# Kernel optimization log

Hardware: AMD Instinct MI355X
Metric: run time of the kernel (lower is better)

The kernel has to match this reference:

```python
import jax, jax.numpy as jnp
import numpy as np

N = 12                      # matrix size (input_size)
TRI = N * (N + 1) // 2      # 78 lower-triangular entries
HID = 512
BATCH = 262144


def setup_inputs() -> dict:
    key = jax.random.key(0)
    ks = jax.random.split(key, 4)
    s1 = 1.0 / np.sqrt(N)
    s2 = 1.0 / np.sqrt(HID)
    return {
        "x": jax.random.normal(ks[0], (BATCH, N), dtype=jnp.float32),
        "W1": jax.random.normal(ks[1], (N, HID), dtype=jnp.float32) * s1,
        "b1": jnp.zeros((HID,), dtype=jnp.float32),
        "W2": jax.random.normal(ks[2], (HID, HID), dtype=jnp.float32) * s2,
        "b2": jnp.zeros((HID,), dtype=jnp.float32),
        "W3": jax.random.normal(ks[3], (HID, TRI + 1), dtype=jnp.float32) * s2,
        "b3": jnp.zeros((TRI + 1,), dtype=jnp.float32),
    }


def reference(x, W1, b1, W2, b2, W3, b3):
    # 3-layer MLP (assumed parent-class structure): relu, relu, softplus
    h = jax.nn.relu(x @ W1 + b1)
    h = jax.nn.relu(h @ W2 + b2)
    out = jax.nn.softplus(h @ W3 + b3)          # [B, TRI+1]
    # Vectorized row-major lower-triangular scatter (replaces nested python loop)
    rows, cols = jnp.tril_indices(N)            # row-major order matches idx loop
    B = x.shape[0]
    L = jnp.zeros((B, N, N), dtype=out.dtype).at[:, rows, cols].set(out[:, :TRI])
    MMT = jnp.einsum('bij,bkj->bik', L, L)      # M @ M^T, PSD [B, N, N]
    c = out[:, TRI]                             # [B]
    return MMT, c
```

## Files before the change

kernel.cpp:

```cpp
#include <hip/hip_runtime.h>
#include <math.h>

typedef __attribute__((ext_vector_type(8))) _Float16 fp16x8;
typedef __attribute__((ext_vector_type(4))) _Float16 fp16x4;
typedef __attribute__((ext_vector_type(2))) __fp16 hfp16x2;
typedef __attribute__((ext_vector_type(4))) __fp16 hfp16x4;
typedef __attribute__((ext_vector_type(4))) float floatx4;

#define HID 512
#define TRIC 78
#define OUTC 79
#define BATCH 262144
#define HPAD 520
#define OPAD 84
#define XPAD 24
#define X_OFF 33280

#define W2P_OFF 16384
#define W3P_OFF 278528

__global__ __launch_bounds__(256) void prep_kernel(const float* __restrict__ W1,
                                                   const float* __restrict__ W2,
                                                   const float* __restrict__ W3,
                                                   _Float16* __restrict__ wsh) {
  int g = blockIdx.x * 256 + threadIdx.x;
  int lane = g & 63;
  int l15 = lane & 15, q = lane >> 4;
  fp16x8 v;
  if (g < 2048) {
    int ct = g >> 6;
    int c = ct * 16 + l15;
#pragma unroll
    for (int j = 0; j < 8; ++j) {
      int k = q * 8 + j;
      v[j] = (k < 12) ? (_Float16)W1[k * HID + c] : (_Float16)0.f;
    }
    *(fp16x8*)(wsh + (size_t)g * 8) = v;
  } else if (g < 34816) {
    int h = g - 2048;
    int fk = h >> 6;
    int kb = fk & 15, ct = fk >> 4;
    int c = ct * 16 + l15;
    int kbase = kb * 32 + q * 8;
#pragma unroll
    for (int j = 0; j < 8; ++j) v[j] = (_Float16)W2[(kbase + j) * HID + c];
    *(fp16x8*)(wsh + W2P_OFF + (size_t)h * 8) = v;
  } else if (g < 39936) {
    int h = g - 34816;
    int fk = h >> 6;
    int kb = fk & 15, ct = fk >> 4;
    int c = ct * 16 + l15;
    int kbase = kb * 32 + q * 8;
#pragma unroll
    for (int j = 0; j < 8; ++j)
      v[j] = (c < OUTC) ? (_Float16)W3[(kbase + j) * OUTC + c] : (_Float16)0.f;
    *(fp16x8*)(wsh + W3P_OFF + (size_t)h * 8) = v;
  }
}

__device__ __forceinline__ float softplus_f(float v) {
  float e = __expf(-fabsf(v));
  return fmaxf(v, 0.f) + __logf(1.f + e);
}

__device__ __forceinline__ fp16x4 relu_pk4(floatx4 a) {
  hfp16x2 lo = __builtin_amdgcn_cvt_pkrtz(fmaxf(a[0], 0.f), fmaxf(a[1], 0.f));
  hfp16x2 hi = __builtin_amdgcn_cvt_pkrtz(fmaxf(a[2], 0.f), fmaxf(a[3], 0.f));
  hfp16x4 r = __builtin_shufflevector(lo, hi, 0, 1, 2, 3);
  return __builtin_bit_cast(fp16x4, r);
}

__global__ __launch_bounds__(512, 4) void fused_kernel(const float* __restrict__ x,
                                                       const float* __restrict__ b1,
                                                       const float* __restrict__ b2,
                                                       const float* __restrict__ b3,
                                                       const _Float16* __restrict__ wsh,
                                                       float* __restrict__ out) {
  __shared__ __align__(16) _Float16 hbuf[X_OFF + 64 * XPAD];
  const int tid = threadIdx.x;
  const int wave = tid >> 6, lane = tid & 63;
  const int l15 = lane & 15, quad = lane >> 4;
  const int r0 = blockIdx.x * 64;

  const fp16x8* w1p = (const fp16x8*)wsh;
  const fp16x8* w2p = (const fp16x8*)(wsh + W2P_OFF);
  const fp16x8* w3p = (const fp16x8*)(wsh + W3P_OFF);

  {
    _Float16* xs = hbuf + X_OFF;
    const float* xg = x + (size_t)r0 * 12;
    if (tid < 256) {
      int e = 512 + tid;
      int row = e / 12, col = e - row * 12;
      xs[row * XPAD + col] = (_Float16)xg[e];
      xs[(tid >> 2) * XPAD + 12 + (tid & 3)] = (_Float16)0.f;
    }
    {
      int row = tid / 12, col = tid - row * 12;
      xs[row * XPAD + col] = (_Float16)xg[tid];
    }
  }
  fp16x8 a1p[4];
#pragma unroll
  for (int ct = 0; ct < 4; ++ct) a1p[ct] = w1p[(wave * 4 + ct) * 64 + lane];
  __syncthreads();

  fp16x8 zf;
#pragma unroll
  for (int j = 0; j < 8; ++j) zf[j] = (_Float16)0.f;

  floatx4 bq[4];
#pragma unroll
  for (int ct = 0; ct < 4; ++ct)
    bq[ct] = *(const floatx4*)(b1 + wave * 64 + ct * 16 + quad * 4);

  floatx4 acc[4][4];
#pragma unroll
  for (int ct = 0; ct < 4; ++ct)
#pragma unroll
    for (int nt = 0; nt < 4; ++nt) acc[ct][nt] = bq[ct];

  {
    const _Float16* xs = hbuf + X_OFF;
    fp16x8 xb[4];
#pragma unroll
    for (int nt = 0; nt < 4; ++nt)
      xb[nt] = (quad < 2) ? *(const fp16x8*)(xs + (nt * 16 + l15) * XPAD + quad * 8) : zf;
#pragma unroll
    for (int ct = 0; ct < 4; ++ct) {
#pragma unroll
      for (int nt = 0; nt < 4; ++nt)
        acc[ct][nt] = __builtin_amdgcn_mfma_f32_16x16x32_f16(a1p[ct], xb[nt], acc[ct][nt], 0, 0, 0);
    }
  }

#pragma unroll
  for (int ct = 0; ct < 4; ++ct)
#pragma unroll
    for (int nt = 0; nt < 4; ++nt)
      *(fp16x4*)(hbuf + (nt * 16 + l15) * HPAD + wave * 64 + ct * 16 + quad * 4) =
          relu_pk4(acc[ct][nt]);
  fp16x8 ap[4];
#pragma unroll
  for (int ct = 0; ct < 4; ++ct) ap[ct] = w2p[((wave * 4 + ct) * 16 + 0) * 64 + lane];
  __syncthreads();

#pragma unroll
  for (int ct = 0; ct < 4; ++ct)
    bq[ct] = *(const floatx4*)(b2 + wave * 64 + ct * 16 + quad * 4);
#pragma unroll
  for (int ct = 0; ct < 4; ++ct)
#pragma unroll
    for (int nt = 0; nt < 4; ++nt) acc[ct][nt] = bq[ct];

#pragma unroll 2
  for (int kb = 0; kb < 16; ++kb) {
    fp16x8 a[4], b[4];
#pragma unroll
    for (int ct = 0; ct < 4; ++ct) a[ct] = ap[ct];
#pragma unroll
    for (int nt = 0; nt < 4; ++nt)
      b[nt] = *(const fp16x8*)(hbuf + (nt * 16 + l15) * HPAD + kb * 32 + quad * 8);
    const int kbn = (kb + 1) & 15;
#pragma unroll
    for (int ct = 0; ct < 4; ++ct) ap[ct] = w2p[((wave * 4 + ct) * 16 + kbn) * 64 + lane];
    __builtin_amdgcn_s_setprio(1);
#pragma unroll
    for (int ct = 0; ct < 4; ++ct)
#pragma unroll
      for (int nt = 0; nt < 4; ++nt)
        acc[ct][nt] = __builtin_amdgcn_mfma_f32_16x16x32_f16(a[ct], b[nt], acc[ct][nt], 0, 0, 0);
    __builtin_amdgcn_s_setprio(0);
  }

  __syncthreads();

#pragma unroll
  for (int ct = 0; ct < 4; ++ct)
#pragma unroll
    for (int nt = 0; nt < 4; ++nt)
      *(fp16x4*)(hbuf + (nt * 16 + l15) * HPAD + wave * 64 + ct * 16 + quad * 4) =
          relu_pk4(acc[ct][nt]);

  const int mt3 = wave >> 1;
  const int codd = wave & 1;
  const int c0 = codd ? 3 : 0;
  const int nct = codd ? 2 : 3;

  floatx4 b3q[3];
#pragma unroll
  for (int j = 0; j < 3; ++j) {
#pragma unroll
    for (int r = 0; r < 4; ++r) {
      int c = (c0 + j) * 16 + quad * 4 + r;
      b3q[j][r] = (j < nct && c < OUTC) ? b3[c] : 0.f;
    }
  }
  floatx4 acc3[3];
#pragma unroll
  for (int j = 0; j < 3; ++j) acc3[j] = b3q[j];

  fp16x8 ap3[3];
#pragma unroll
  for (int j = 0; j < 3; ++j) ap3[j] = zf;
#pragma unroll
  for (int j = 0; j < 3; ++j)
    if (j < nct) ap3[j] = w3p[((c0 + j) * 16 + 0) * 64 + lane];
  __syncthreads();

#pragma unroll 2
  for (int kb = 0; kb < 16; ++kb) {
    fp16x8 bfrag = *(const fp16x8*)(hbuf + (mt3 * 16 + l15) * HPAD + kb * 32 + quad * 8);
    fp16x8 a3[3];
#pragma unroll
    for (int j = 0; j < 3; ++j) a3[j] = ap3[j];
    const int kbn = (kb + 1) & 15;
#pragma unroll
    for (int j = 0; j < 3; ++j)
      if (j < nct) ap3[j] = w3p[((c0 + j) * 16 + kbn) * 64 + lane];
    __builtin_amdgcn_s_setprio(1);
#pragma unroll
    for (int j = 0; j < 3; ++j)
      if (j < nct)
        acc3[j] = __builtin_amdgcn_mfma_f32_16x16x32_f16(a3[j], bfrag, acc3[j], 0, 0, 0);
    __builtin_amdgcn_s_setprio(0);
  }
  __syncthreads();

  float* outf = (float*)hbuf;
#pragma unroll
  for (int j = 0; j < 3; ++j)
    if (j < nct) {
      floatx4 v;
#pragma unroll
      for (int r = 0; r < 4; ++r) v[r] = softplus_f(acc3[j][r]);
      *(floatx4*)(outf + (mt3 * 16 + l15) * OPAD + (c0 + j) * 16 + quad * 4) = v;
    }
  if (codd && quad == 3)
    out[(size_t)BATCH * 144 + r0 + mt3 * 16 + l15] = softplus_f(acc3[1][2]);
  __syncthreads();

  {
    const float* Lbase = (const float*)hbuf;
    const int rowl = tid >> 3;
    const int sub = tid & 7;
    const float* Lr = Lbase + rowl * OPAD;

    float R[80];
#pragma unroll
    for (int q = 0; q < 20; ++q) {
      floatx4 v = *(const floatx4*)(Lr + q * 4);
#pragma unroll
      for (int r = 0; r < 4; ++r) R[q * 4 + r] = v[r];
    }

    float Lj0[12], Lj1[12];
    {
      const int tj = (sub * (sub + 1)) >> 1;
#pragma unroll
      for (int k = 0; k < 12; ++k) Lj0[k] = (k <= sub) ? Lr[tj + k] : 0.f;
#pragma unroll
      for (int k = 0; k < 12; ++k) Lj1[k] = 0.f;
      const int j1 = sub + 8;
      if (sub < 4) {
        const int tj1 = (j1 * (j1 + 1)) >> 1;
#pragma unroll
        for (int k = 0; k < 12; ++k) Lj1[k] = (k <= j1) ? Lr[tj1 + k] : 0.f;
      }
    }

    float* Mg = out + ((size_t)r0 + rowl) * 144;
#pragma unroll
    for (int i = 0; i < 12; ++i) {
      const int ti = (i * (i + 1)) >> 1;
      float s0 = 0.f, s1 = 0.f;
#pragma unroll
      for (int k = 0; k <= i; ++k) {
        const float li = R[ti + k];
        s0 = fmaf(li, Lj0[k], s0);
        s1 = fmaf(li, Lj1[k], s1);
      }
      Mg[i * 12 + sub] = s0;
      if (sub < 4) Mg[i * 12 + sub + 8] = s1;
    }
  }
}

extern "C" void kernel_launch(void* const* d_in, const int* in_sizes, int n_in,
                              void* d_out, int out_size, void* d_ws, size_t ws_size,
                              hipStream_t stream) {
  const float* x  = (const float*)d_in[0];
  const float* W1 = (const float*)d_in[1];
  const float* b1 = (const float*)d_in[2];
  const float* W2 = (const float*)d_in[3];
  const float* b2 = (const float*)d_in[4];
  const float* W3 = (const float*)d_in[5];
  const float* b3 = (const float*)d_in[6];
  float* out = (float*)d_out;
  _Float16* wsh = (_Float16*)d_ws;

  prep_kernel<<<156, 256, 0, stream>>>(W1, W2, W3, wsh);
  fused_kernel<<<BATCH / 64, 512, 0, stream>>>(x, b1, b2, b3, wsh, out);
}
```

Baseline: 344.6 us.

## Double rows per block to 128 and reshape per-wave MFMA tiles

```diff
diff --git a/kernel.cpp b/kernel.cpp
--- a/kernel.cpp
+++ b/kernel.cpp
@@ -11,10 +11,11 @@
 #define TRIC 78
 #define OUTC 79
 #define BATCH 262144
+#define ROWS 128
 #define HPAD 520
 #define OPAD 84
 #define XPAD 24
-#define X_OFF 33280
+#define X_OFF 66560
 
 #define W2P_OFF 16384
 #define W3P_OFF 278528
@@ -70,17 +71,17 @@
   return __builtin_bit_cast(fp16x4, r);
 }
 
-__global__ __launch_bounds__(512, 4) void fused_kernel(const float* __restrict__ x,
-                                                       const float* __restrict__ b1,
-                                                       const float* __restrict__ b2,
-                                                       const float* __restrict__ b3,
-                                                       const _Float16* __restrict__ wsh,
-                                                       float* __restrict__ out) {
-  __shared__ __align__(16) _Float16 hbuf[X_OFF + 64 * XPAD];
+__global__ __launch_bounds__(1024, 4) void fused_kernel(const float* __restrict__ x,
+                                                        const float* __restrict__ b1,
+                                                        const float* __restrict__ b2,
+                                                        const float* __restrict__ b3,
+                                                        const _Float16* __restrict__ wsh,
+                                                        float* __restrict__ out) {
+  __shared__ __align__(16) _Float16 hbuf[X_OFF + ROWS * XPAD];
   const int tid = threadIdx.x;
   const int wave = tid >> 6, lane = tid & 63;
   const int l15 = lane & 15, quad = lane >> 4;
-  const int r0 = blockIdx.x * 64;
+  const int r0 = blockIdx.x * ROWS;
 
   const fp16x8* w1p = (const fp16x8*)wsh;
   const fp16x8* w2p = (const fp16x8*)(wsh + W2P_OFF);
@@ -89,97 +90,85 @@
   {
     _Float16* xs = hbuf + X_OFF;
     const float* xg = x + (size_t)r0 * 12;
-    if (tid < 256) {
-      int e = 512 + tid;
+    {
+      int row = tid / 12, col = tid - row * 12;
+      xs[row * XPAD + col] = (_Float16)xg[tid];
+    }
+    if (tid < 512) {
+      int e = 1024 + tid;
       int row = e / 12, col = e - row * 12;
       xs[row * XPAD + col] = (_Float16)xg[e];
       xs[(tid >> 2) * XPAD + 12 + (tid & 3)] = (_Float16)0.f;
     }
-    {
-      int row = tid / 12, col = tid - row * 12;
-      xs[row * XPAD + col] = (_Float16)xg[tid];
-    }
-  }
-  fp16x8 a1p[4];
-#pragma unroll
-  for (int ct = 0; ct < 4; ++ct) a1p[ct] = w1p[(wave * 4 + ct) * 64 + lane];
+  }
+  fp16x8 a1p[2];
+#pragma unroll
+  for (int ct = 0; ct < 2; ++ct) a1p[ct] = w1p[(wave * 2 + ct) * 64 + lane];
   __syncthreads();
 
   fp16x8 zf;
 #pragma unroll
   for (int j = 0; j < 8; ++j) zf[j] = (_Float16)0.f;
 
-  floatx4 bq[4];
-#pragma unroll
-  for (int ct = 0; ct < 4; ++ct)
-    bq[ct] = *(const floatx4*)(b1 + wave * 64 + ct * 16 + quad * 4);
-
-  floatx4 acc[4][4];
-#pragma unroll
-  for (int ct = 0; ct < 4; ++ct)
-#pragma unroll
-    for (int nt = 0; nt < 4; ++nt) acc[ct][nt] = bq[ct];
+  floatx4 acc[2][8];
+#pragma unroll
+  for (int ct = 0; ct < 2; ++ct) {
+    floatx4 bqc = *(const floatx4*)(b1 + wave * 32 + ct * 16 + quad * 4);
+#pragma unroll
+    for (int nt = 0; nt < 8; ++nt) acc[ct][nt] = bqc;
+  }
 
   {
     const _Float16* xs = hbuf + X_OFF;
-    fp16x8 xb[4];
-#pragma unroll
-    for (int nt = 0; nt < 4; ++nt)
-      xb[nt] = (quad < 2) ? *(const fp16x8*)(xs + (nt * 16 + l15) * XPAD + quad * 8) : zf;
-#pragma unroll
-    for (int ct = 0; ct < 4; ++ct) {
-#pragma unroll
-      for (int nt = 0; nt < 4; ++nt)
-        acc[ct][nt] = __builtin_amdgcn_mfma_f32_16x16x32_f16(a1p[ct], xb[nt], acc[ct][nt], 0, 0, 0);
-    }
-  }
-
-#pragma unroll
-  for (int ct = 0; ct < 4; ++ct)
-#pragma unroll
-    for (int nt = 0; nt < 4; ++nt)
-      *(fp16x4*)(hbuf + (nt * 16 + l15) * HPAD + wave * 64 + ct * 16 + quad * 4) =
+#pragma unroll
+    for (int nt = 0; nt < 8; ++nt) {
+      fp16x8 xb = (quad < 2) ? *(const fp16x8*)(xs + (nt * 16 + l15) * XPAD + quad * 8) : zf;
+      acc[0][nt] = __builtin_amdgcn_mfma_f32_16x16x32_f16(a1p[0], xb, acc[0][nt], 0, 0, 0);
+      acc[1][nt] = __builtin_amdgcn_mfma_f32_16x16x32_f16(a1p[1], xb, acc[1][nt], 0, 0, 0);
+    }
+  }
+
+#pragma unroll
+  for (int ct = 0; ct < 2; ++ct)
+#pragma unroll
+    for (int nt = 0; nt < 8; ++nt)
+      *(fp16x4*)(hbuf + (nt * 16 + l15) * HPAD + wave * 32 + ct * 16 + quad * 4) =
           relu_pk4(acc[ct][nt]);
-  fp16x8 ap[4];
-#pragma unroll
-  for (int ct = 0; ct < 4; ++ct) ap[ct] = w2p[((wave * 4 + ct) * 16 + 0) * 64 + lane];
-  __syncthreads();
-
-#pragma unroll
-  for (int ct = 0; ct < 4; ++ct)
-    bq[ct] = *(const floatx4*)(b2 + wave * 64 + ct * 16 + quad * 4);
-#pragma unroll
-  for (int ct = 0; ct < 4; ++ct)
-#pragma unroll
-    for (int nt = 0; nt < 4; ++nt) acc[ct][nt] = bq[ct];
+  fp16x8 ap[2];
+#pragma unroll
+  for (int ct = 0; ct < 2; ++ct) ap[ct] = w2p[((wave * 2 + ct) * 16 + 0) * 64 + lane];
+  __syncthreads();
+
+#pragma unroll
+  for (int ct = 0; ct < 2; ++ct) {
+    floatx4 bqc = *(const floatx4*)(b2 + wave * 32 + ct * 16 + quad * 4);
+#pragma unroll
+    for (int nt = 0; nt < 8; ++nt) acc[ct][nt] = bqc;
+  }
 
 #pragma unroll 2
   for (int kb = 0; kb < 16; ++kb) {
-    fp16x8 a[4], b[4];
-#pragma unroll
-    for (int ct = 0; ct < 4; ++ct) a[ct] = ap[ct];
-#pragma unroll
-    for (int nt = 0; nt < 4; ++nt)
-      b[nt] = *(const fp16x8*)(hbuf + (nt * 16 + l15) * HPAD + kb * 32 + quad * 8);
+    fp16x8 a0 = ap[0], a1v = ap[1];
     const int kbn = (kb + 1) & 15;
-#pragma unroll
-    for (int ct = 0; ct < 4; ++ct) ap[ct] = w2p[((wave * 4 + ct) * 16 + kbn) * 64 + lane];
+    ap[0] = w2p[((wave * 2 + 0) * 16 + kbn) * 64 + lane];
+    ap[1] = w2p[((wave * 2 + 1) * 16 + kbn) * 64 + lane];
     __builtin_amdgcn_s_setprio(1);
 #pragma unroll
-    for (int ct = 0; ct < 4; ++ct)
-#pragma unroll
-      for (int nt = 0; nt < 4; ++nt)
-        acc[ct][nt] = __builtin_amdgcn_mfma_f32_16x16x32_f16(a[ct], b[nt], acc[ct][nt], 0, 0, 0);
+    for (int nt = 0; nt < 8; ++nt) {
+      fp16x8 b = *(const fp16x8*)(hbuf + (nt * 16 + l15) * HPAD + kb * 32 + quad * 8);
+      acc[0][nt] = __builtin_amdgcn_mfma_f32_16x16x32_f16(a0, b, acc[0][nt], 0, 0, 0);
+      acc[1][nt] = __builtin_amdgcn_mfma_f32_16x16x32_f16(a1v, b, acc[1][nt], 0, 0, 0);
+    }
     __builtin_amdgcn_s_setprio(0);
   }
 
   __syncthreads();
 
 #pragma unroll
-  for (int ct = 0; ct < 4; ++ct)
-#pragma unroll
-    for (int nt = 0; nt < 4; ++nt)
-      *(fp16x4*)(hbuf + (nt * 16 + l15) * HPAD + wave * 64 + ct * 16 + quad * 4) =
+  for (int ct = 0; ct < 2; ++ct)
+#pragma unroll
+    for (int nt = 0; nt < 8; ++nt)
+      *(fp16x4*)(hbuf + (nt * 16 + l15) * HPAD + wave * 32 + ct * 16 + quad * 4) =
           relu_pk4(acc[ct][nt]);
 
   const int mt3 = wave >> 1;
@@ -300,5 +289,5 @@
   _Float16* wsh = (_Float16*)d_ws;
 
   prep_kernel<<<156, 256, 0, stream>>>(W1, W2, W3, wsh);
-  fused_kernel<<<BATCH / 64, 512, 0, stream>>>(x, b1, b2, b3, wsh, out);
-}
+  fused_kernel<<<BATCH / ROWS, 1024, 0, stream>>>(x, b1, b2, b3, wsh, out);
+}
```

After: 349.8 us. About the same (+1.5%).
